# Kernel tuning notes

Measured on AMD Instinct MI355X. Metric: run time of the kernel, lower is better.

Reference implementation:

```python
import jax, jax.numpy as jnp
import numpy as np

N = 100000   # nodes
E = 640000   # edges
F = 128      # num_features
H = 128      # hidden_channels
EPS = 1e-5   # BatchNorm1d eps
SCALE = 0.05


def setup_inputs() -> dict:
    key = jax.random.key(0)
    ks = jax.random.split(key, 16)
    inp = {
        "x": jax.random.normal(ks[0], (N, F), dtype=jnp.float32),
        "edge_index": jax.random.randint(ks[1], (2, E), 0, N, dtype=jnp.int32),
    }
    dims = [(F, H), (H, H), (H, H)]
    k = 2
    for i, (din, dout) in enumerate(dims):
        inp[f"Wl{i}"] = jax.random.normal(ks[k], (dout, din), dtype=jnp.float32) * SCALE
        inp[f"bl{i}"] = jax.random.normal(ks[k + 1], (dout,), dtype=jnp.float32) * SCALE
        inp[f"Wr{i}"] = jax.random.normal(ks[k + 2], (dout, din), dtype=jnp.float32) * SCALE
        k += 3
    inp["W1"] = jax.random.normal(ks[k], (H, H), dtype=jnp.float32) * SCALE
    inp["b1"] = jax.random.normal(ks[k + 1], (H,), dtype=jnp.float32) * SCALE
    inp["W2"] = jax.random.normal(ks[k + 2], (2, H), dtype=jnp.float32) * SCALE
    inp["b2"] = jax.random.normal(ks[k + 3], (2,), dtype=jnp.float32) * SCALE
    return inp


def _batchnorm(x):
    # BatchNorm1d(track_running_stats=False, affine=False): biased batch stats
    mu = jnp.mean(x, axis=0)
    var = jnp.var(x, axis=0)
    return (x - mu) / jnp.sqrt(var + EPS)


def _sage_conv(x, src, dst, Wl, bl, Wr):
    # PyG SAGEConv (aggr='mean'): out = lin_l(mean_agg(x[src] -> dst)) + lin_r(x)
    msg = x[src]                                             # [E, din]
    ssum = jax.ops.segment_sum(msg, dst, num_segments=N)     # [N, din]
    cnt = jax.ops.segment_sum(jnp.ones((E,), x.dtype), dst, num_segments=N)
    agg = ssum / jnp.maximum(cnt, 1.0)[:, None]              # mean, 0 for isolated
    return agg @ Wl.T + bl + x @ Wr.T


def reference(x, edge_index, Wl0, bl0, Wr0, Wl1, bl1, Wr1, Wl2, bl2, Wr2, W1, b1, W2, b2):
    src, dst = edge_index[0], edge_index[1]
    for Wl, bl, Wr in ((Wl0, bl0, Wr0), (Wl1, bl1, Wr1), (Wl2, bl2, Wr2)):
        x = jax.nn.relu(_batchnorm(_sage_conv(x, src, dst, Wl, bl, Wr)))
    x = jax.nn.relu(_batchnorm(x @ W1.T + b1))
    return x @ W2.T + b2
```

## Files before the change

### kernel.cpp

```cpp
#include <hip/hip_runtime.h>
#include <stdint.h>

typedef __bf16 v8bf __attribute__((ext_vector_type(8)));
typedef float f32x4 __attribute__((ext_vector_type(4)));
typedef float f32x2 __attribute__((ext_vector_type(2)));

__device__ __forceinline__ float b2f(unsigned short u) {
    unsigned int x = ((unsigned int)u) << 16;
    return __builtin_bit_cast(float, x);
}
__device__ __forceinline__ float b2f_lo(unsigned int v) {
    return __builtin_bit_cast(float, v << 16);
}
__device__ __forceinline__ float b2f_hi(unsigned int v) {
    return __builtin_bit_cast(float, v & 0xffff0000u);
}
__device__ __forceinline__ unsigned short f2b(float f) {
    unsigned int x = __builtin_bit_cast(unsigned int, f);
    unsigned int r = (x + 0x7fffu + ((x >> 16) & 1u)) >> 16;
    return (unsigned short)r;
}

__device__ __forceinline__ void load_lds16(const void* g, void* l) {
    __builtin_amdgcn_global_load_lds(
        (__attribute__((address_space(1))) void*)(const void*)g,
        (__attribute__((address_space(3))) void*)l, 16, 0, 0);
}

__device__ __forceinline__ void barrier_raw() {
    __builtin_amdgcn_sched_barrier(0);
    __builtin_amdgcn_s_barrier();
    __builtin_amdgcn_sched_barrier(0);
}

#define VMW(n) asm volatile("s_waitcnt vmcnt(" #n ")" ::: "memory")

struct WSrc { const float* p[7]; const float* s[6]; };

__global__ void k_prologue(WSrc w, unsigned short* __restrict__ wbuf,
                           const int* __restrict__ src, const int* __restrict__ dst,
                           int* __restrict__ pos, int* __restrict__ csr, int E,
                           const float* __restrict__ x, unsigned short* __restrict__ xcat,
                           unsigned short* __restrict__ y,
                           int n, int nFill, int nCvtw, int nCopyx) {
    int bid = blockIdx.x;
    int t = threadIdx.x;
    if (bid < nFill) {
        int i = bid * 256 + t;
        if (i < E) {
            int d = dst[i];
            int p = atomicAdd(&pos[d], 1);
            if (p < 64) csr[((size_t)d << 6) + p] = src[i];
        }
    } else if (bid < nFill + nCvtw) {
        int idx = (bid - nFill) * 256 + t;
        if (idx < 115458) {
            float v;
            if (idx < 114688) {
                v = w.p[idx >> 14][idx & 16383];
            } else {
                int rem = idx - 114688;
                int tt, j;
                if (rem < 512)      { tt = rem >> 7; j = rem & 127; }
                else if (rem < 768) { tt = 4; j = rem - 512; }
                else                { tt = 5; j = rem - 768; }
                v = w.s[tt][j];
            }
            wbuf[idx] = f2b(v);
        } else if (idx < 115458 + 64) {
            int k = idx - 115458;
            if (k < 32) {
                ushort4 z; z.x = z.y = z.z = z.w = 0;
                *(ushort4*)&xcat[(size_t)n * 256 + 128 + k * 4] = z;
            } else {
                ushort4 m; m.x = m.y = m.z = m.w = 0xFF7Fu;
                *(ushort4*)&y[(size_t)n * 128 + (k - 32) * 4] = m;
            }
        }
    } else {
        int T = nCopyx * 256;
        int tid = (bid - nFill - nCvtw) * 256 + t;
        int total = n * 32;
        for (int i0 = tid; i0 < total; i0 += 4 * T) {
#pragma unroll
            for (int u = 0; u < 4; u++) {
                int i = i0 + u * T;
                if (i < total) {
                    int row = i >> 5, c4 = (i & 31) * 4;
                    float4 v = *(const float4*)&x[(size_t)row * 128 + c4];
                    ushort4 o;
                    o.x = f2b(v.x); o.y = f2b(v.y); o.z = f2b(v.z); o.w = f2b(v.w);
                    *(ushort4*)&xcat[(size_t)row * 256 + 128 + c4] = o;
                }
            }
        }
    }
}

__global__ void k_hist(const int* __restrict__ pos, int* __restrict__ hist, int n) {
    __shared__ int lh[32];
    int t = threadIdx.x;
    int i = blockIdx.x * 256 + t;
    if (t < 32) lh[t] = 0;
    __syncthreads();
    if (i < n) atomicAdd(&lh[31 - min(pos[i], 31)], 1);
    __syncthreads();
    if (t < 32) atomicAdd(&hist[t], lh[t]);
}

__global__ void k_order(const int* __restrict__ cnt, const int* __restrict__ hist,
                        int* __restrict__ binpos, int* __restrict__ order, int n) {
    __shared__ int lh[32], gb[32], hloc[32];
    int t = threadIdx.x;
    if (t < 32) { lh[t] = 0; hloc[t] = hist[t]; }
    __syncthreads();
    int i = blockIdx.x * 256 + t;
    int b = 0, r = 0;
    if (i < n) {
        b = 31 - min(cnt[i], 31);
        r = atomicAdd(&lh[b], 1);
    }
    __syncthreads();
    if (t < 32) {
        int off = 0;
        for (int k = 0; k < t; k++) off += hloc[k];
        gb[t] = off + atomicAdd(&binpos[t], lh[t]);
    }
    __syncthreads();
    if (i < n) order[gb[b] + r] = i;
}

__global__ __launch_bounds__(256) void k_agg(const unsigned short* __restrict__ xcat,
                                             const int* __restrict__ cnt, const int* __restrict__ csr,
                                             const int* __restrict__ order,
                                             unsigned short* __restrict__ outL, int n) {
    int t = threadIdx.x;
    int l = t & 15;
    int gbase = (t & 63) & ~15;
    int oi = blockIdx.x * 16 + (t >> 4);
    if (oi >= n) return;
    int d = order[oi];
    size_t s = (size_t)d << 6;
    int deg = cnt[d];
    f32x2 ax[4] = {};
    for (int base = 0; base < deg; base += 16) {
        int myidx = (base + l < deg) ? csr[s + base + l] : n;
        int lim = min(16, deg - base);
        for (int b = 0; b < lim; b += 8) {
            int idx[8];
            uint4 v[8];
#pragma unroll
            for (int u = 0; u < 8; u++) idx[u] = __shfl(myidx, gbase + b + u, 64);
#pragma unroll
            for (int u = 0; u < 8; u++)
                v[u] = *(const uint4*)(xcat + (((unsigned)idx[u]) << 8) + 128u + (unsigned)(l << 3));
#pragma unroll
            for (int u = 0; u < 8; u++) {
                unsigned int uu[4] = {v[u].x, v[u].y, v[u].z, v[u].w};
#pragma unroll
                for (int k = 0; k < 4; k++) {
                    f32x2 tv;
                    tv.x = b2f_lo(uu[k]);
                    tv.y = b2f_hi(uu[k]);
                    ax[k] += tv;
                }
            }
        }
    }
    float ic = 1.0f / (float)max(deg, 1);
    uint4 o;
    unsigned int* op = (unsigned int*)&o;
#pragma unroll
    for (int k = 0; k < 4; k++)
        op[k] = ((unsigned int)f2b(ax[k].y * ic) << 16) | f2b(ax[k].x * ic);
    *(uint4*)&outL[(size_t)d * 256 + l * 8] = o;
}

__global__ __launch_bounds__(256) void k_aggbn(const unsigned short* __restrict__ Y,
                                               const float* __restrict__ statp,
                                               const int* __restrict__ cnt, const int* __restrict__ csr,
                                               const int* __restrict__ order,
                                               unsigned short* __restrict__ xcat, int n, float invN) {
    __shared__ float smu[128], sinv[128], sq[128];
    int t = threadIdx.x;
    if (t < 128) {
        float s = 0.f;
#pragma unroll
        for (int sl = 0; sl < 32; sl++) s += statp[sl * 256 + t];
        smu[t] = s * invN;
    } else {
        int u = t - 128;
        float q = 0.f;
#pragma unroll
        for (int sl = 0; sl < 32; sl++) q += statp[sl * 256 + 128 + u];
        sq[u] = q;
    }
    __syncthreads();
    if (t < 128) {
        float mu = smu[t];
        sinv[t] = rsqrtf(sq[t] * invN - mu * mu + 1e-5f);
    }
    __syncthreads();
    int l = t & 15;
    int gbase = (t & 63) & ~15;
    int oi = blockIdx.x * 16 + (t >> 4);
    if (oi >= n) return;
    int d = order[oi];
    f32x2 mu2[4];
    float iv[8];
#pragma unroll
    for (int k = 0; k < 4; k++) {
        mu2[k].x = smu[l * 8 + 2 * k];
        mu2[k].y = smu[l * 8 + 2 * k + 1];
    }
#pragma unroll
    for (int k = 0; k < 8; k++) iv[k] = sinv[l * 8 + k];
    {
        uint4 vo = *(const uint4*)&Y[(size_t)oi * 128 + l * 8];
        unsigned int uu[4] = {vo.x, vo.y, vo.z, vo.w};
        uint4 o;
        unsigned int* op = (unsigned int*)&o;
#pragma unroll
        for (int k = 0; k < 4; k++) {
            float a = fmaxf((b2f_lo(uu[k]) - mu2[k].x) * iv[2 * k], 0.f);
            float b = fmaxf((b2f_hi(uu[k]) - mu2[k].y) * iv[2 * k + 1], 0.f);
            op[k] = ((unsigned int)f2b(b) << 16) | f2b(a);
        }
        *(uint4*)&xcat[(size_t)oi * 256 + 128 + l * 8] = o;
    }
    size_t s = (size_t)d << 6;
    int deg = cnt[d];
    f32x2 z2 = {0.f, 0.f};
    f32x2 ax[4] = {};
    for (int base = 0; base < deg; base += 16) {
        int myidx = (base + l < deg) ? csr[s + base + l] : n;
        int lim = min(16, deg - base);
        for (int b = 0; b < lim; b += 8) {
            int idx[8];
            uint4 v[8];
#pragma unroll
            for (int u = 0; u < 8; u++) idx[u] = __shfl(myidx, gbase + b + u, 64);
#pragma unroll
            for (int u = 0; u < 8; u++)
                v[u] = *(const uint4*)(Y + (((unsigned)idx[u]) << 7) + (unsigned)(l << 3));
#pragma unroll
            for (int u = 0; u < 8; u++) {
                unsigned int uu[4] = {v[u].x, v[u].y, v[u].z, v[u].w};
#pragma unroll
                for (int k = 0; k < 4; k++) {
                    f32x2 tv;
                    tv.x = b2f_lo(uu[k]);
                    tv.y = b2f_hi(uu[k]);
                    tv = tv - mu2[k];
                    tv = __builtin_elementwise_max(tv, z2);
                    ax[k] += tv;
                }
            }
        }
    }
    float ic = 1.0f / (float)max(deg, 1);
    uint4 o;
    unsigned int* op = (unsigned int*)&o;
#pragma unroll
    for (int k = 0; k < 4; k++)
        op[k] = ((unsigned int)f2b(ax[k].y * (iv[2 * k + 1] * ic)) << 16)
              | f2b(ax[k].x * (iv[2 * k] * ic));
    *(uint4*)&xcat[(size_t)d * 256 + l * 8] = o;
}

template<int NCH>
__global__ __launch_bounds__(256) void k_wgemm(const unsigned short* __restrict__ A, int lda, int aoff,
                                               const unsigned short* __restrict__ W0,
                                               const unsigned short* __restrict__ W1,
                                               const unsigned short* __restrict__ bias,
                                               unsigned short* __restrict__ Y,
                                               float* __restrict__ statp, int nrows) {
    constexpr int HALF = NCH / 2;
    constexpr int LPH = HALF / 2;
    __shared__ __align__(16) unsigned short Ws[NCH][4096];
    __shared__ __align__(16) unsigned short As[2][HALF][1024];
    int t = threadIdx.x;
    int wv = t >> 6, lane = t & 63;
    int quad = lane >> 4, l16 = lane & 15;

    for (int c = 0; c < NCH; c++) {
        const unsigned short* Wp = (c < 4) ? W0 : W1;
        int wkc = (c & 3) * 32;
#pragma unroll
        for (int q = 0; q < 2; q++) {
            int r = q * 64 + (t >> 2);
            load_lds16(Wp + (size_t)r * 128 + wkc + (t & 3) * 8,
                       &Ws[c][(size_t)r * 32 + (t & 3) * 8]);
        }
    }

    float bn[2][4];
#pragma unroll
    for (int j = 0; j < 2; j++) {
        int c0 = wv * 32 + j * 16 + quad * 4;
        uint2 bu = *(const uint2*)&bias[c0];
        bn[j][0] = b2f_lo(bu.x); bn[j][1] = b2f_hi(bu.x);
        bn[j][2] = b2f_lo(bu.y); bn[j][3] = b2f_hi(bu.y);
    }

    f32x4 cs_[2] = {}, cq_[2] = {};

    int ntiles = (nrows + 31) >> 5;
    int tt = t & 127;
    int half = t >> 7;
    int ar = tt >> 2, ac = (tt & 3) * 8;

    auto stage = [&](int m0, int hb, int buf) {
#pragma unroll
        for (int p2 = 0; p2 < LPH; p2++) {
            int slot = p2 * 2 + half;
            int gr = m0 + ar;
            if (gr >= nrows) gr = nrows - 1;
            load_lds16(A + (size_t)gr * lda + aoff + (hb + slot) * 32 + ac,
                       &As[buf][slot][(size_t)ar * 32 + ac]);
        }
    };
    auto compute_half = [&](int hb, int buf, f32x4 (&acc)[2][2]) {
#pragma unroll
        for (int c = 0; c < HALF; c++) {
            v8bf af[2], bfv[2];
#pragma unroll
            for (int i = 0; i < 2; i++)
                af[i] = *(const v8bf*)&As[buf][c][(i * 16 + l16) * 32 + quad * 8];
#pragma unroll
            for (int j = 0; j < 2; j++)
                bfv[j] = *(const v8bf*)&Ws[hb + c][(wv * 32 + j * 16 + l16) * 32 + quad * 8];
#pragma unroll
            for (int i = 0; i < 2; i++)
#pragma unroll
                for (int j = 0; j < 2; j++)
                    acc[i][j] = __builtin_amdgcn_mfma_f32_16x16x32_bf16(bfv[j], af[i], acc[i][j], 0, 0, 0);
        }
    };

    int mt = blockIdx.x;
    stage(mt * 32, 0, 0);
    stage(mt * 32, HALF, 1);
    bool first = true;
    for (; mt < ntiles; mt += (int)gridDim.x) {
        int m0 = mt * 32;
        int nxt = mt + (int)gridDim.x;
        int nm0 = (nxt < ntiles) ? nxt * 32 : m0;

        if (first) {
            if constexpr (LPH == 2) VMW(2); else VMW(1);
        } else {
            if constexpr (LPH == 2) VMW(6); else VMW(5);
        }
        barrier_raw();

        f32x4 acc[2][2] = {};
        compute_half(0, 0, acc);
        barrier_raw();
        stage(nm0, 0, 0);

        if constexpr (LPH == 2) VMW(2); else VMW(1);
        barrier_raw();
        compute_half(HALF, 1, acc);

#pragma unroll
        for (int i = 0; i < 2; i++)
#pragma unroll
            for (int j = 0; j < 2; j++)
#pragma unroll
                for (int u = 0; u < 4; u++)
                    acc[i][j][u] += bn[j][u];
#pragma unroll
        for (int i = 0; i < 2; i++) {
            int row = m0 + i * 16 + l16;
            int srow = (row < nrows) ? row : (nrows + 1);
#pragma unroll
            for (int j = 0; j < 2; j++) {
                int c0 = wv * 32 + j * 16 + quad * 4;
                uint2 o;
                o.x = ((unsigned int)f2b(acc[i][j][1]) << 16) | f2b(acc[i][j][0]);
                o.y = ((unsigned int)f2b(acc[i][j][3]) << 16) | f2b(acc[i][j][2]);
                *(uint2*)&Y[(size_t)srow * 128 + c0] = o;
            }
        }
#pragma unroll
        for (int i = 0; i < 2; i++) {
            int row = m0 + i * 16 + l16;
            if (row < nrows) {
#pragma unroll
                for (int j = 0; j < 2; j++)
#pragma unroll
                    for (int u = 0; u < 4; u++) {
                        float v = acc[i][j][u];
                        cs_[j][u] += v;
                        cq_[j][u] += v * v;
                    }
            }
        }
        barrier_raw();
        stage(nm0, HALF, 1);
        first = false;
    }

    float* sp = statp + (blockIdx.x & 31) * 256;
#pragma unroll
    for (int j = 0; j < 2; j++) {
        for (int m = 1; m < 16; m <<= 1) {
#pragma unroll
            for (int u = 0; u < 4; u++) {
                cs_[j][u] += __shfl_xor(cs_[j][u], m, 64);
                cq_[j][u] += __shfl_xor(cq_[j][u], m, 64);
            }
        }
        if (l16 == 0) {
            int c0 = wv * 32 + j * 16 + quad * 4;
#pragma unroll
            for (int u = 0; u < 4; u++) {
                atomicAdd(&sp[c0 + u], cs_[j][u]);
                atomicAdd(&sp[128 + c0 + u], cq_[j][u]);
            }
        }
    }
}

__global__ __launch_bounds__(256) void k_wgemm_bn(const unsigned short* __restrict__ A,
                                                  const float* __restrict__ statp,
                                                  const unsigned short* __restrict__ W0,
                                                  const unsigned short* __restrict__ bias,
                                                  unsigned short* __restrict__ Y,
                                                  float* __restrict__ statp_out,
                                                  int nrows, float invN) {
    __shared__ __align__(16) unsigned short Ws[4][4096];
    __shared__ __align__(16) unsigned short As[4][1024];
    __shared__ float smu[128], sinv[128], sq[128];
    int t = threadIdx.x;
    int wv = t >> 6, lane = t & 63;
    int quad = lane >> 4, l16 = lane & 15;

    for (int c = 0; c < 4; c++) {
        int wkc = c * 32;
#pragma unroll
        for (int q = 0; q < 2; q++) {
            int r = q * 64 + (t >> 2);
            load_lds16(W0 + (size_t)r * 128 + wkc + (t & 3) * 8,
                       &Ws[c][(size_t)r * 32 + (t & 3) * 8]);
        }
    }

    if (t < 128) {
        float s = 0.f;
#pragma unroll
        for (int sl = 0; sl < 32; sl++) s += statp[sl * 256 + t];
        smu[t] = s * invN;
    } else {
        int u = t - 128;
        float q = 0.f;
#pragma unroll
        for (int sl = 0; sl < 32; sl++) q += statp[sl * 256 + 128 + u];
        sq[u] = q;
    }
    __syncthreads();
    if (t < 128) {
        float mu = smu[t];
        sinv[t] = rsqrtf(sq[t] * invN - mu * mu + 1e-5f);
    }
    __syncthreads();

    int c16 = (t & 15) * 8;
    int sch = (t & 15) >> 2;
    int sac = (t & 3) * 8;
    int sr = t >> 4;
    float mu8[8], iv8[8];
#pragma unroll
    for (int k = 0; k < 8; k++) { mu8[k] = smu[c16 + k]; iv8[k] = sinv[c16 + k]; }

    float bn[2][4];
#pragma unroll
    for (int j = 0; j < 2; j++) {
        int c0 = wv * 32 + j * 16 + quad * 4;
        uint2 bu = *(const uint2*)&bias[c0];
        bn[j][0] = b2f_lo(bu.x); bn[j][1] = b2f_hi(bu.x);
        bn[j][2] = b2f_lo(bu.y); bn[j][3] = b2f_hi(bu.y);
    }

    f32x4 cs_[2] = {}, cq_[2] = {};

    int ntiles = (nrows + 31) >> 5;
    int mt = blockIdx.x;
    uint4 ra0, ra1;
    {
        int g0 = min(mt * 32 + sr, nrows - 1);
        int g1 = min(mt * 32 + 16 + sr, nrows - 1);
        ra0 = *(const uint4*)(A + (size_t)g0 * 128 + c16);
        ra1 = *(const uint4*)(A + (size_t)g1 * 128 + c16);
    }
    auto xf = [&](uint4 v) -> uint4 {
        unsigned int uu[4] = {v.x, v.y, v.z, v.w};
        uint4 o; unsigned int* op = (unsigned int*)&o;
#pragma unroll
        for (int k = 0; k < 4; k++) {
            float a = fmaxf((b2f_lo(uu[k]) - mu8[2 * k]) * iv8[2 * k], 0.f);
            float b = fmaxf((b2f_hi(uu[k]) - mu8[2 * k + 1]) * iv8[2 * k + 1], 0.f);
            op[k] = ((unsigned int)f2b(b) << 16) | f2b(a);
        }
        return o;
    };

    for (; mt < ntiles; mt += (int)gridDim.x) {
        int m0 = mt * 32;
        int nxt = mt + (int)gridDim.x;

        VMW(0);
        barrier_raw();
        *(uint4*)&As[sch][(size_t)sr * 32 + sac] = xf(ra0);
        *(uint4*)&As[sch][(size_t)(16 + sr) * 32 + sac] = xf(ra1);
        __syncthreads();

        if (nxt < ntiles) {
            int g0 = min(nxt * 32 + sr, nrows - 1);
            int g1 = min(nxt * 32 + 16 + sr, nrows - 1);
            ra0 = *(const uint4*)(A + (size_t)g0 * 128 + c16);
            ra1 = *(const uint4*)(A + (size_t)g1 * 128 + c16);
        }

        f32x4 acc[2][2] = {};
#pragma unroll
        for (int c = 0; c < 4; c++) {
            v8bf af[2], bfv[2];
#pragma unroll
            for (int i = 0; i < 2; i++)
                af[i] = *(const v8bf*)&As[c][(i * 16 + l16) * 32 + quad * 8];
#pragma unroll
            for (int j = 0; j < 2; j++)
                bfv[j] = *(const v8bf*)&Ws[c][(wv * 32 + j * 16 + l16) * 32 + quad * 8];
#pragma unroll
            for (int i = 0; i < 2; i++)
#pragma unroll
                for (int j = 0; j < 2; j++)
                    acc[i][j] = __builtin_amdgcn_mfma_f32_16x16x32_bf16(bfv[j], af[i], acc[i][j], 0, 0, 0);
        }

#pragma unroll
        for (int i = 0; i < 2; i++)
#pragma unroll
            for (int j = 0; j < 2; j++)
#pragma unroll
                for (int u = 0; u < 4; u++)
                    acc[i][j][u] += bn[j][u];
#pragma unroll
        for (int i = 0; i < 2; i++) {
            int row = m0 + i * 16 + l16;
            int srow = (row < nrows) ? row : (nrows + 1);
#pragma unroll
            for (int j = 0; j < 2; j++) {
                int c0 = wv * 32 + j * 16 + quad * 4;
                uint2 o;
                o.x = ((unsigned int)f2b(acc[i][j][1]) << 16) | f2b(acc[i][j][0]);
                o.y = ((unsigned int)f2b(acc[i][j][3]) << 16) | f2b(acc[i][j][2]);
                *(uint2*)&Y[(size_t)srow * 128 + c0] = o;
            }
        }
#pragma unroll
        for (int i = 0; i < 2; i++) {
            int row = m0 + i * 16 + l16;
            if (row < nrows) {
#pragma unroll
                for (int j = 0; j < 2; j++)
#pragma unroll
                    for (int u = 0; u < 4; u++) {
                        float v = acc[i][j][u];
                        cs_[j][u] += v;
                        cq_[j][u] += v * v;
                    }
            }
        }
    }

    float* sp = statp_out + (blockIdx.x & 31) * 256;
#pragma unroll
    for (int j = 0; j < 2; j++) {
        for (int m = 1; m < 16; m <<= 1) {
#pragma unroll
            for (int u = 0; u < 4; u++) {
                cs_[j][u] += __shfl_xor(cs_[j][u], m, 64);
                cq_[j][u] += __shfl_xor(cq_[j][u], m, 64);
            }
        }
        if (l16 == 0) {
            int c0 = wv * 32 + j * 16 + quad * 4;
#pragma unroll
            for (int u = 0; u < 4; u++) {
                atomicAdd(&sp[c0 + u], cs_[j][u]);
                atomicAdd(&sp[128 + c0 + u], cq_[j][u]);
            }
        }
    }
}

__global__ __launch_bounds__(256) void k_bnfinal(const unsigned short* __restrict__ Y,
                                                 const float* __restrict__ statp,
                                                 const unsigned short* __restrict__ W2,
                                                 const unsigned short* __restrict__ b2v,
                                                 float* __restrict__ out, int n, float invN) {
    __shared__ float smu[128], sinv[128], sq[128];
    int t = threadIdx.x;
    if (t < 128) {
        float s = 0.f;
#pragma unroll
        for (int sl = 0; sl < 32; sl++) s += statp[sl * 256 + t];
        smu[t] = s * invN;
    } else {
        int u = t - 128;
        float q = 0.f;
#pragma unroll
        for (int sl = 0; sl < 32; sl++) q += statp[sl * 256 + 128 + u];
        sq[u] = q;
    }
    __syncthreads();
    if (t < 128) {
        float mu = smu[t];
        sinv[t] = rsqrtf(sq[t] * invN - mu * mu + 1e-5f);
    }
    __syncthreads();
    int wid = t >> 6, lane = t & 63;
    int r = blockIdx.x * 4 + wid;
    if (r >= n) return;
    int f2 = lane * 2;
    unsigned int v = *(const unsigned int*)&Y[(size_t)r * 128 + f2];
    float a = fmaxf((b2f_lo(v) - smu[f2]) * sinv[f2], 0.f);
    float b = fmaxf((b2f_hi(v) - smu[f2 + 1]) * sinv[f2 + 1], 0.f);
    unsigned int w0 = *(const unsigned int*)&W2[f2];
    unsigned int w1 = *(const unsigned int*)&W2[128 + f2];
    float d0 = a * b2f_lo(w0) + b * b2f_hi(w0);
    float d1 = a * b2f_lo(w1) + b * b2f_hi(w1);
    for (int o = 32; o > 0; o >>= 1) {
        d0 += __shfl_down(d0, o, 64);
        d1 += __shfl_down(d1, o, 64);
    }
    if (lane == 0) {
        float2 o2;
        o2.x = d0 + b2f(b2v[0]);
        o2.y = d1 + b2f(b2v[1]);
        *(float2*)&out[(size_t)r * 2] = o2;
    }
}

extern "C" void kernel_launch(void* const* d_in, const int* in_sizes, int n_in,
                              void* d_out, int out_size, void* d_ws, size_t ws_size,
                              hipStream_t stream) {
    const int N = in_sizes[0] / 128;
    const int E = in_sizes[1] / 2;

    const float* x = (const float*)d_in[0];
    const int* ei = (const int*)d_in[1];
    const int* srcp = ei;
    const int* dstp = ei + E;
    float* out = (float*)d_out;

    char* w = (char*)d_ws;
    auto align256 = [](size_t v) { return (v + 255) & ~(size_t)255; };
    size_t o_xcat = 0;
    size_t o_y    = align256(o_xcat + (size_t)(N + 1) * 256 * 2);
    size_t o_csr  = align256(o_y + (size_t)(N + 2) * 128 * 2);
    size_t o_ord  = align256(o_csr + (size_t)N * 64 * 4);
    size_t o_wbuf = align256(o_ord + (size_t)N * 4);
    size_t o_pos  = align256(o_wbuf + 115712 * 2);
    size_t o_stat = o_pos + (size_t)N * 4;
    size_t o_hist = o_stat + 4 * 8192 * 4;
    size_t o_binp = o_hist + 32 * 4;

    unsigned short* xcat = (unsigned short*)(w + o_xcat);
    unsigned short* y    = (unsigned short*)(w + o_y);
    int* csr = (int*)(w + o_csr);
    int* ord  = (int*)(w + o_ord);
    unsigned short* wbuf = (unsigned short*)(w + o_wbuf);
    int* pos = (int*)(w + o_pos);
    float* stat = (float*)(w + o_stat);
    int* hist = (int*)(w + o_hist);
    int* binp = (int*)(w + o_binp);

    const unsigned short* Wl[3] = {wbuf + 0,      wbuf + 32768, wbuf + 65536};
    const unsigned short* Wr[3] = {wbuf + 16384,  wbuf + 49152, wbuf + 81920};
    const unsigned short* W1b   = wbuf + 98304;
    const unsigned short* bl[3] = {wbuf + 114688, wbuf + 114816, wbuf + 114944};
    const unsigned short* b1b   = wbuf + 115072;
    const unsigned short* W2b   = wbuf + 115200;
    const unsigned short* b2b   = wbuf + 115456;

    WSrc wsrc;
    wsrc.p[0] = (const float*)d_in[2];
    wsrc.p[1] = (const float*)d_in[4];
    wsrc.p[2] = (const float*)d_in[5];
    wsrc.p[3] = (const float*)d_in[7];
    wsrc.p[4] = (const float*)d_in[8];
    wsrc.p[5] = (const float*)d_in[10];
    wsrc.p[6] = (const float*)d_in[11];
    wsrc.s[0] = (const float*)d_in[3];
    wsrc.s[1] = (const float*)d_in[6];
    wsrc.s[2] = (const float*)d_in[9];
    wsrc.s[3] = (const float*)d_in[12];
    wsrc.s[4] = (const float*)d_in[13];
    wsrc.s[5] = (const float*)d_in[14];

    const int NB = (N + 255) / 256;
    const int nFill = (E + 255) / 256;
    const int nCvtw = (115458 + 64 + 255) / 256;
    const int nCopyx = 1024;

    hipMemsetAsync(w + o_pos, 0, (size_t)N * 4 + 4 * 8192 * 4 + 64 * 4, stream);

    k_prologue<<<nFill + nCvtw + nCopyx, 256, 0, stream>>>(wsrc, wbuf, srcp, dstp, pos, csr, E,
                                                           x, xcat, y, N, nFill, nCvtw, nCopyx);
    k_hist<<<NB, 256, 0, stream>>>(pos, hist, N);
    k_order<<<NB, 256, 0, stream>>>(pos, hist, binp, ord, N);

    const int wg_grid = 512;
    const int agg16_grid = (N + 15) / 16;
    const int wave_grid = (N + 3) / 4;
    const float invN = 1.0f / (float)N;

    k_agg<<<agg16_grid, 256, 0, stream>>>(xcat, pos, csr, ord, xcat, N);
    k_wgemm<8><<<wg_grid, 256, 0, stream>>>(xcat, 256, 0, Wl[0], Wr[0], bl[0], y, stat + 0 * 8192, N);
    for (int i = 1; i < 3; i++) {
        k_aggbn<<<agg16_grid, 256, 0, stream>>>(y, stat + (i - 1) * 8192, pos, csr, ord, xcat, N, invN);
        k_wgemm<8><<<wg_grid, 256, 0, stream>>>(xcat, 256, 0, Wl[i], Wr[i], bl[i], y, stat + i * 8192, N);
    }
    k_wgemm_bn<<<wg_grid, 256, 0, stream>>>(y, stat + 2 * 8192, W1b, b1b, y, stat + 3 * 8192, N, invN);
    k_bnfinal<<<wave_grid, 256, 0, stream>>>(y, stat + 3 * 8192, W2b, b2b, out, N, invN);
}
```

Measured before the change: 370.7 us.

## Hold GEMM weights in registers, raise occupancy, vectorize final BN head

k_wgemm now keeps its weight fragments in VGPRs instead of staging all 8 weight chunks into LDS. This cuts LDS use from about 80KB to 16KB, allowing 3 blocks per CU, and the grid grows from 512 to 768 blocks. k_bnfinal now has 16 lanes per row with 16-byte loads and 16 rows per block, replacing one wave per row. The risk is extra register pressure in the GEMM (16 v8bf weight registers per thread) and possible spills under the 3-block launch bound.

```diff
diff --git a/kernel.cpp b/kernel.cpp
--- a/kernel.cpp
+++ b/kernel.cpp
@@ -268,30 +268,37 @@
     *(uint4*)&xcat[(size_t)d * 256 + l * 8] = o;
 }
 
-template<int NCH>
-__global__ __launch_bounds__(256) void k_wgemm(const unsigned short* __restrict__ A, int lda, int aoff,
-                                               const unsigned short* __restrict__ W0,
-                                               const unsigned short* __restrict__ W1,
-                                               const unsigned short* __restrict__ bias,
-                                               unsigned short* __restrict__ Y,
-                                               float* __restrict__ statp, int nrows) {
-    constexpr int HALF = NCH / 2;
-    constexpr int LPH = HALF / 2;
-    __shared__ __align__(16) unsigned short Ws[NCH][4096];
-    __shared__ __align__(16) unsigned short As[2][HALF][1024];
+#define MFMA4(HB, BUF)                                                              \
+    do {                                                                            \
+        _Pragma("unroll")                                                           \
+        for (int c = 0; c < 4; c++) {                                               \
+            v8bf af0 = *(const v8bf*)&As[BUF][c][(l16) * 32 + quad * 8];            \
+            v8bf af1 = *(const v8bf*)&As[BUF][c][(16 + l16) * 32 + quad * 8];       \
+            acc[0][0] = __builtin_amdgcn_mfma_f32_16x16x32_bf16(wreg[(HB) + c][0], af0, acc[0][0], 0, 0, 0); \
+            acc[0][1] = __builtin_amdgcn_mfma_f32_16x16x32_bf16(wreg[(HB) + c][1], af0, acc[0][1], 0, 0, 0); \
+            acc[1][0] = __builtin_amdgcn_mfma_f32_16x16x32_bf16(wreg[(HB) + c][0], af1, acc[1][0], 0, 0, 0); \
+            acc[1][1] = __builtin_amdgcn_mfma_f32_16x16x32_bf16(wreg[(HB) + c][1], af1, acc[1][1], 0, 0, 0); \
+        }                                                                           \
+    } while (0)
+
+__global__ __launch_bounds__(256, 3) void k_wgemm(const unsigned short* __restrict__ A, int lda, int aoff,
+                                                  const unsigned short* __restrict__ W0,
+                                                  const unsigned short* __restrict__ W1,
+                                                  const unsigned short* __restrict__ bias,
+                                                  unsigned short* __restrict__ Y,
+                                                  float* __restrict__ statp, int nrows) {
+    __shared__ __align__(16) unsigned short As[2][4][1024];
     int t = threadIdx.x;
     int wv = t >> 6, lane = t & 63;
     int quad = lane >> 4, l16 = lane & 15;
 
-    for (int c = 0; c < NCH; c++) {
+    v8bf wreg[8][2];
+#pragma unroll
+    for (int c = 0; c < 8; c++) {
         const unsigned short* Wp = (c < 4) ? W0 : W1;
-        int wkc = (c & 3) * 32;
-#pragma unroll
-        for (int q = 0; q < 2; q++) {
-            int r = q * 64 + (t >> 2);
-            load_lds16(Wp + (size_t)r * 128 + wkc + (t & 3) * 8,
-                       &Ws[c][(size_t)r * 32 + (t & 3) * 8]);
-        }
+#pragma unroll
+        for (int j = 0; j < 2; j++)
+            wreg[c][j] = *(const v8bf*)(Wp + (size_t)(wv * 32 + j * 16 + l16) * 128 + (c & 3) * 32 + quad * 8);
     }
 
     float bn[2][4];
@@ -312,7 +319,7 @@
 
     auto stage = [&](int m0, int hb, int buf) {
 #pragma unroll
-        for (int p2 = 0; p2 < LPH; p2++) {
+        for (int p2 = 0; p2 < 2; p2++) {
             int slot = p2 * 2 + half;
             int gr = m0 + ar;
             if (gr >= nrows) gr = nrows - 1;
@@ -320,48 +327,27 @@
                        &As[buf][slot][(size_t)ar * 32 + ac]);
         }
     };
-    auto compute_half = [&](int hb, int buf, f32x4 (&acc)[2][2]) {
-#pragma unroll
-        for (int c = 0; c < HALF; c++) {
-            v8bf af[2], bfv[2];
-#pragma unroll
-            for (int i = 0; i < 2; i++)
-                af[i] = *(const v8bf*)&As[buf][c][(i * 16 + l16) * 32 + quad * 8];
-#pragma unroll
-            for (int j = 0; j < 2; j++)
-                bfv[j] = *(const v8bf*)&Ws[hb + c][(wv * 32 + j * 16 + l16) * 32 + quad * 8];
-#pragma unroll
-            for (int i = 0; i < 2; i++)
-#pragma unroll
-                for (int j = 0; j < 2; j++)
-                    acc[i][j] = __builtin_amdgcn_mfma_f32_16x16x32_bf16(bfv[j], af[i], acc[i][j], 0, 0, 0);
-        }
-    };
 
     int mt = blockIdx.x;
     stage(mt * 32, 0, 0);
-    stage(mt * 32, HALF, 1);
+    stage(mt * 32, 4, 1);
     bool first = true;
     for (; mt < ntiles; mt += (int)gridDim.x) {
         int m0 = mt * 32;
         int nxt = mt + (int)gridDim.x;
         int nm0 = (nxt < ntiles) ? nxt * 32 : m0;
 
-        if (first) {
-            if constexpr (LPH == 2) VMW(2); else VMW(1);
-        } else {
-            if constexpr (LPH == 2) VMW(6); else VMW(5);
-        }
+        if (first) { VMW(2); } else { VMW(6); }
         barrier_raw();
 
         f32x4 acc[2][2] = {};
-        compute_half(0, 0, acc);
+        MFMA4(0, 0);
         barrier_raw();
         stage(nm0, 0, 0);
 
-        if constexpr (LPH == 2) VMW(2); else VMW(1);
+        VMW(2);
         barrier_raw();
-        compute_half(HALF, 1, acc);
+        MFMA4(4, 1);
 
 #pragma unroll
         for (int i = 0; i < 2; i++)
@@ -398,7 +384,7 @@
             }
         }
         barrier_raw();
-        stage(nm0, HALF, 1);
+        stage(nm0, 4, 1);
         first = false;
     }
 
@@ -622,22 +608,30 @@
         sinv[t] = rsqrtf(sq[t] * invN - mu * mu + 1e-5f);
     }
     __syncthreads();
-    int wid = t >> 6, lane = t & 63;
-    int r = blockIdx.x * 4 + wid;
+    int l = t & 15;
+    int r = blockIdx.x * 16 + (t >> 4);
     if (r >= n) return;
-    int f2 = lane * 2;
-    unsigned int v = *(const unsigned int*)&Y[(size_t)r * 128 + f2];
-    float a = fmaxf((b2f_lo(v) - smu[f2]) * sinv[f2], 0.f);
-    float b = fmaxf((b2f_hi(v) - smu[f2 + 1]) * sinv[f2 + 1], 0.f);
-    unsigned int w0 = *(const unsigned int*)&W2[f2];
-    unsigned int w1 = *(const unsigned int*)&W2[128 + f2];
-    float d0 = a * b2f_lo(w0) + b * b2f_hi(w0);
-    float d1 = a * b2f_lo(w1) + b * b2f_hi(w1);
-    for (int o = 32; o > 0; o >>= 1) {
-        d0 += __shfl_down(d0, o, 64);
-        d1 += __shfl_down(d1, o, 64);
-    }
-    if (lane == 0) {
+    int f8 = l * 8;
+    uint4 v = *(const uint4*)&Y[(size_t)r * 128 + f8];
+    uint4 w0v = *(const uint4*)&W2[f8];
+    uint4 w1v = *(const uint4*)&W2[128 + f8];
+    unsigned int uu[4] = {v.x, v.y, v.z, v.w};
+    unsigned int u0[4] = {w0v.x, w0v.y, w0v.z, w0v.w};
+    unsigned int u1[4] = {w1v.x, w1v.y, w1v.z, w1v.w};
+    float d0 = 0.f, d1 = 0.f;
+#pragma unroll
+    for (int k = 0; k < 4; k++) {
+        int f = f8 + 2 * k;
+        float a = fmaxf((b2f_lo(uu[k]) - smu[f]) * sinv[f], 0.f);
+        float b = fmaxf((b2f_hi(uu[k]) - smu[f + 1]) * sinv[f + 1], 0.f);
+        d0 += a * b2f_lo(u0[k]) + b * b2f_hi(u0[k]);
+        d1 += a * b2f_lo(u1[k]) + b * b2f_hi(u1[k]);
+    }
+    for (int o = 1; o < 16; o <<= 1) {
+        d0 += __shfl_xor(d0, o, 64);
+        d1 += __shfl_xor(d1, o, 64);
+    }
+    if (l == 0) {
         float2 o2;
         o2.x = d0 + b2f(b2v[0]);
         o2.y = d1 + b2f(b2v[1]);
@@ -714,17 +708,17 @@
     k_hist<<<NB, 256, 0, stream>>>(pos, hist, N);
     k_order<<<NB, 256, 0, stream>>>(pos, hist, binp, ord, N);
 
-    const int wg_grid = 512;
+    const int wg_grid = 768;
     const int agg16_grid = (N + 15) / 16;
-    const int wave_grid = (N + 3) / 4;
+    const int row16_grid = (N + 15) / 16;
     const float invN = 1.0f / (float)N;
 
     k_agg<<<agg16_grid, 256, 0, stream>>>(xcat, pos, csr, ord, xcat, N);
-    k_wgemm<8><<<wg_grid, 256, 0, stream>>>(xcat, 256, 0, Wl[0], Wr[0], bl[0], y, stat + 0 * 8192, N);
+    k_wgemm<<<wg_grid, 256, 0, stream>>>(xcat, 256, 0, Wl[0], Wr[0], bl[0], y, stat + 0 * 8192, N);
     for (int i = 1; i < 3; i++) {
         k_aggbn<<<agg16_grid, 256, 0, stream>>>(y, stat + (i - 1) * 8192, pos, csr, ord, xcat, N, invN);
-        k_wgemm<8><<<wg_grid, 256, 0, stream>>>(xcat, 256, 0, Wl[i], Wr[i], bl[i], y, stat + i * 8192, N);
-    }
-    k_wgemm_bn<<<wg_grid, 256, 0, stream>>>(y, stat + 2 * 8192, W1b, b1b, y, stat + 3 * 8192, N, invN);
-    k_bnfinal<<<wave_grid, 256, 0, stream>>>(y, stat + 3 * 8192, W2b, b2b, out, N, invN);
-}
+        k_wgemm<<<wg_grid, 256, 0, stream>>>(xcat, 256, 0, Wl[i], Wr[i], bl[i], y, stat + i * 8192, N);
+    }
+    k_wgemm_bn<<<512, 256, 0, stream>>>(y, stat + 2 * 8192, W1b, b1b, y, stat + 3 * 8192, N, invN);
+    k_bnfinal<<<row16_grid, 256, 0, stream>>>(y, stat + 3 * 8192, W2b, b2b, out, N, invN);
+}
```

New measurement: 353.6 us. -4.6%, faster.
